# Optimization experiments

Measured on AMD Instinct MI355X. Metric: run time of the kernel, lower is better.

The kernel has to match this reference:

```python
import jax, jax.numpy as jnp
import numpy as np

N_NODES = 10000
N_EDGES = 640000
IN_FEATS = 256
H_FEATS = 128
NUM_CLASSES = 64


def _kaiming(key, shape):
    fan_in = shape[1]
    std = np.sqrt(2.0 / fan_in)
    return jax.random.normal(key, shape, dtype=jnp.float32) * std


def setup_inputs() -> dict:
    key = jax.random.key(0)
    ks = jax.random.split(key, 10)
    x = jax.random.normal(ks[0], (N_NODES, IN_FEATS), dtype=jnp.float32)
    edge_index = jax.random.randint(ks[1], (2, N_EDGES), 0, N_NODES, dtype=jnp.int64)
    return {
        "x": x,
        "edge_index": edge_index,
        "W_lin": _kaiming(ks[2], (H_FEATS, IN_FEATS)),
        "b_lin": jnp.zeros((H_FEATS,), jnp.float32),
        "Wl1": _kaiming(ks[3], (H_FEATS, H_FEATS)),
        "bl1": jnp.zeros((H_FEATS,), jnp.float32),
        "Wr1": _kaiming(ks[4], (H_FEATS, H_FEATS)),
        "Wl2": _kaiming(ks[5], (H_FEATS, H_FEATS)),
        "bl2": jnp.zeros((H_FEATS,), jnp.float32),
        "Wr2": _kaiming(ks[6], (H_FEATS, H_FEATS)),
        "W_cls": _kaiming(ks[7], (NUM_CLASSES, H_FEATS)),
    }


def _sage_conv(x, src, dst, Wl, bl, Wr, n_nodes):
    # PyG SAGEConv (mean aggr): out = lin_l(mean_{j->i} x_j) + lin_r(x_i)
    msg = x[src]                                    # [E, H] gather
    agg = jax.ops.segment_sum(msg, dst, num_segments=n_nodes)  # [N, H]
    deg = jax.ops.segment_sum(jnp.ones((src.shape[0],), x.dtype), dst,
                              num_segments=n_nodes)            # [N]
    mean = agg / jnp.maximum(deg, 1.0)[:, None]
    return mean @ Wl.T + bl + x @ Wr.T


def reference(x, edge_index, W_lin, b_lin, Wl1, bl1, Wr1, Wl2, bl2, Wr2, W_cls):
    src, dst = edge_index[0], edge_index[1]
    n = x.shape[0]
    h = jax.nn.relu(x @ W_lin.T + b_lin)            # input projection + relu
    h = _sage_conv(h, src, dst, Wl1, bl1, Wr1, n)   # sage1 (no relu: linear is truthy)
    h = _sage_conv(h, src, dst, Wl2, bl2, Wr2, n)   # sage2
    h = jax.nn.relu(h)
    return h @ W_cls.T                              # weight.mm(x.t()).t()
```

## Files before the change

### kernel.cpp

```cpp
#include <hip/hip_runtime.h>

#define NN 10000
#define HF 128
#define INF_ 256
#define CLS 64
#define CAP 128
#define RT  (NN / 16)

typedef __attribute__((ext_vector_type(8))) short short8;
typedef __attribute__((ext_vector_type(4))) float f32x4;

__device__ __forceinline__ unsigned short f2bf(float f) {
    unsigned u = __builtin_bit_cast(unsigned, f);
    u = (u + 0x7fffu + ((u >> 16) & 1u)) >> 16;
    return (unsigned short)u;
}
__device__ __forceinline__ float bfbits2f(unsigned u) {
    u <<= 16;
    return __builtin_bit_cast(float, u);
}


template <int K>
__device__ __forceinline__
void mfma_acc(int row_tile, int col0,
              const unsigned short* __restrict__ A,
              const unsigned short* __restrict__ W, f32x4 acc[4]) {
    int lane = threadIdx.x & 63;
    int m = lane & 15, quad = lane >> 4;
    const short8* ap  = (const short8*)(A + (size_t)(row_tile * 16 + m) * K + quad * 8);
    const short8* bp0 = (const short8*)(W + (size_t)(col0 +  0 + m) * K + quad * 8);
    const short8* bp1 = (const short8*)(W + (size_t)(col0 + 16 + m) * K + quad * 8);
    const short8* bp2 = (const short8*)(W + (size_t)(col0 + 32 + m) * K + quad * 8);
    const short8* bp3 = (const short8*)(W + (size_t)(col0 + 48 + m) * K + quad * 8);
#pragma unroll
    for (int k0 = 0; k0 < K; k0 += 32) {
        int ki = k0 >> 3;
        short8 a = ap[ki];
        acc[0] = __builtin_amdgcn_mfma_f32_16x16x32_bf16(a, bp0[ki], acc[0], 0, 0, 0);
        acc[1] = __builtin_amdgcn_mfma_f32_16x16x32_bf16(a, bp1[ki], acc[1], 0, 0, 0);
        acc[2] = __builtin_amdgcn_mfma_f32_16x16x32_bf16(a, bp2[ki], acc[2], 0, 0, 0);
        acc[3] = __builtin_amdgcn_mfma_f32_16x16x32_bf16(a, bp3[ki], acc[3], 0, 0, 0);
    }
}

template <bool OUT_BF16, bool RELU_OUT, bool HAS_BIAS, bool HAS_TMP>
__device__ __forceinline__
void epilogue4(int row_tile, int col0, int N, const float* __restrict__ bias,
               const float* __restrict__ tmp, f32x4 acc[4], void* __restrict__ out) {
    int lane = threadIdx.x & 63;
    int m = lane & 15, quad = lane >> 4;
#pragma unroll
    for (int c = 0; c < 4; ++c) {
        int colg = col0 + c * 16 + m;
        float bv = HAS_BIAS ? bias[colg] : 0.f;
#pragma unroll
        for (int r = 0; r < 4; ++r) {
            int rowg = row_tile * 16 + quad * 4 + r;
            float v = acc[c][r] + bv;
            if (HAS_TMP) v += tmp[(size_t)rowg * N + colg];
            if (RELU_OUT) v = fmaxf(v, 0.f);
            if (OUT_BF16) ((unsigned short*)out)[(size_t)rowg * N + colg] = f2bf(v);
            else          ((float*)out)[(size_t)rowg * N + colg] = v;
        }
    }
}

__device__ __forceinline__ short8 pack8(float4 a, float4 b) {
    short8 r;
    r[0] = (short)f2bf(a.x); r[1] = (short)f2bf(a.y);
    r[2] = (short)f2bf(a.z); r[3] = (short)f2bf(a.w);
    r[4] = (short)f2bf(b.x); r[5] = (short)f2bf(b.y);
    r[6] = (short)f2bf(b.z); r[7] = (short)f2bf(b.w);
    return r;
}

__device__ __forceinline__
void gemm1_wave(int row_tile, int col0, const float* __restrict__ x,
                const float* __restrict__ Wlin, const float* __restrict__ blin,
                unsigned short* __restrict__ h0) {
    int lane = threadIdx.x & 63;
    int m = lane & 15, quad = lane >> 4;
    const float* ar = x    + (size_t)(row_tile * 16 + m) * INF_ + quad * 8;
    const float* w0 = Wlin + (size_t)(col0 +  0 + m) * INF_ + quad * 8;
    const float* w1 = Wlin + (size_t)(col0 + 16 + m) * INF_ + quad * 8;
    const float* w2 = Wlin + (size_t)(col0 + 32 + m) * INF_ + quad * 8;
    const float* w3 = Wlin + (size_t)(col0 + 48 + m) * INF_ + quad * 8;
    f32x4 acc[4] = {};
#pragma unroll
    for (int k0 = 0; k0 < INF_; k0 += 32) {
        short8 a  = pack8(*(const float4*)(ar + k0), *(const float4*)(ar + k0 + 4));
        short8 b0 = pack8(*(const float4*)(w0 + k0), *(const float4*)(w0 + k0 + 4));
        short8 b1 = pack8(*(const float4*)(w1 + k0), *(const float4*)(w1 + k0 + 4));
        short8 b2 = pack8(*(const float4*)(w2 + k0), *(const float4*)(w2 + k0 + 4));
        short8 b3 = pack8(*(const float4*)(w3 + k0), *(const float4*)(w3 + k0 + 4));
        acc[0] = __builtin_amdgcn_mfma_f32_16x16x32_bf16(a, b0, acc[0], 0, 0, 0);
        acc[1] = __builtin_amdgcn_mfma_f32_16x16x32_bf16(a, b1, acc[1], 0, 0, 0);
        acc[2] = __builtin_amdgcn_mfma_f32_16x16x32_bf16(a, b2, acc[2], 0, 0, 0);
        acc[3] = __builtin_amdgcn_mfma_f32_16x16x32_bf16(a, b3, acc[3], 0, 0, 0);
    }
    epilogue4<true, true, true, false>(row_tile, col0, HF, blin, nullptr, acc, h0);
}

#define GB 313
#define FB 625
#define CB 288

__global__ __launch_bounds__(256)
void fused_k(const float* __restrict__ x, const float* __restrict__ Wlin,
             const float* __restrict__ blin, unsigned short* __restrict__ h0,
             const int* __restrict__ src, const int* __restrict__ dst,
             int* __restrict__ cnt, unsigned short* __restrict__ colb, int E,
             const float* __restrict__ Wl1, const float* __restrict__ Wr1,
             const float* __restrict__ Wl2, const float* __restrict__ Wr2,
             const float* __restrict__ Wcls, unsigned short* __restrict__ wb) {
    int b = blockIdx.x;
    if (b < GB) {
        int wave = threadIdx.x >> 6;
        int row_tile = b * 2 + (wave >> 1);
        if (row_tile >= RT) return;
        gemm1_wave(row_tile, (wave & 1) * 64, x, Wlin, blin, h0);
    } else if (b < GB + FB) {
        int t = (b - GB) * 256 + threadIdx.x;
        if (t * 4 < E) {
            int4 s4 = ((const int4*)src)[t];
            int4 d4 = ((const int4*)dst)[t];
            int p0 = atomicAdd(&cnt[d4.x], 1);
            int p1 = atomicAdd(&cnt[d4.y], 1);
            int p2 = atomicAdd(&cnt[d4.z], 1);
            int p3 = atomicAdd(&cnt[d4.w], 1);
            if (p0 < CAP) colb[(size_t)d4.x * CAP + p0] = (unsigned short)s4.x;
            if (p1 < CAP) colb[(size_t)d4.y * CAP + p1] = (unsigned short)s4.y;
            if (p2 < CAP) colb[(size_t)d4.z * CAP + p2] = (unsigned short)s4.z;
            if (p3 < CAP) colb[(size_t)d4.w * CAP + p3] = (unsigned short)s4.w;
        }
    } else {
        int i = (b - GB - FB) * 256 + threadIdx.x;
        const float* s; int off;
        if      (i < 16384) { s = Wl1;  off = 0; }
        else if (i < 32768) { s = Wr1;  off = 16384; }
        else if (i < 49152) { s = Wl2;  off = 32768; }
        else if (i < 65536) { s = Wr2;  off = 49152; }
        else if (i < 73728) { s = Wcls; off = 65536; }
        else return;
        wb[i] = f2bf(s[i - off]);
    }
}

#define AGB 2500

__global__ __launch_bounds__(256)
void agg_gemm_k(const unsigned short* __restrict__ h, const int* __restrict__ cnt,
                const unsigned short* __restrict__ colb, unsigned short* __restrict__ mv,
                const unsigned short* __restrict__ Wr, float* __restrict__ tmp, int n) {
    int b = blockIdx.x;
    if (b < AGB) {
        int wave = threadIdx.x >> 6;
        int lane = threadIdx.x & 63;
        int q   = lane >> 4;
        int r16 = lane & 15;
        int node = b * 4 + wave;
        if (node >= n) return;
        int deg = cnt[node];
        int c = deg > CAP ? CAP : deg;
        const unsigned short* mycol = colb + (size_t)node * CAP;
        const uint4* __restrict__ hp = (const uint4*)h;

        float a0 = 0.f, a1 = 0.f, a2 = 0.f, a3 = 0.f;
        float a4 = 0.f, a5 = 0.f, a6 = 0.f, a7 = 0.f;
        for (int base = 0; base < c; base += 64) {
            int mm = min(64, c - base);
            int colv = (base + lane < c) ? (int)mycol[base + lane] : 0;
#pragma unroll 4
            for (int jj = 0; jj < 16; ++jj) {
                if (jj * 4 >= mm) break;
                int e = jj * 4 + q;
                int s = __shfl(colv, e);
                if (e < mm) {
                    uint4 v = hp[(size_t)s * 16 + r16];
                    a0 += bfbits2f(v.x & 0xffffu); a1 += bfbits2f(v.x >> 16);
                    a2 += bfbits2f(v.y & 0xffffu); a3 += bfbits2f(v.y >> 16);
                    a4 += bfbits2f(v.z & 0xffffu); a5 += bfbits2f(v.z >> 16);
                    a6 += bfbits2f(v.w & 0xffffu); a7 += bfbits2f(v.w >> 16);
                }
            }
        }
        a0 += __shfl_xor(a0, 16); a0 += __shfl_xor(a0, 32);
        a1 += __shfl_xor(a1, 16); a1 += __shfl_xor(a1, 32);
        a2 += __shfl_xor(a2, 16); a2 += __shfl_xor(a2, 32);
        a3 += __shfl_xor(a3, 16); a3 += __shfl_xor(a3, 32);
        a4 += __shfl_xor(a4, 16); a4 += __shfl_xor(a4, 32);
        a5 += __shfl_xor(a5, 16); a5 += __shfl_xor(a5, 32);
        a6 += __shfl_xor(a6, 16); a6 += __shfl_xor(a6, 32);
        a7 += __shfl_xor(a7, 16); a7 += __shfl_xor(a7, 32);
        if (q == 0) {
            float inv = (deg > 0) ? 1.0f / (float)deg : 0.f;
            uint4 o;
            o.x = (unsigned)f2bf(a0 * inv) | ((unsigned)f2bf(a1 * inv) << 16);
            o.y = (unsigned)f2bf(a2 * inv) | ((unsigned)f2bf(a3 * inv) << 16);
            o.z = (unsigned)f2bf(a4 * inv) | ((unsigned)f2bf(a5 * inv) << 16);
            o.w = (unsigned)f2bf(a6 * inv) | ((unsigned)f2bf(a7 * inv) << 16);
            ((uint4*)mv)[(size_t)node * 16 + r16] = o;
        }
    } else {
        int bb = b - AGB;
        int wave = threadIdx.x >> 6;
        int row_tile = bb * 2 + (wave >> 1);
        if (row_tile >= RT) return;
        int col0 = (wave & 1) * 64;
        f32x4 acc[4] = {};
        mfma_acc<HF>(row_tile, col0, h, Wr, acc);
        epilogue4<false, false, false, false>(row_tile, col0, HF, nullptr, nullptr, acc, tmp);
    }
}

template <bool RELU_OUT>
__global__ __launch_bounds__(256)
void sage_fin_k(const unsigned short* __restrict__ mv, const unsigned short* __restrict__ Wl,
                const float* __restrict__ tmp, const float* __restrict__ bias,
                unsigned short* __restrict__ out) {
    int wave = threadIdx.x >> 6;
    int row_tile = blockIdx.x * 2 + (wave >> 1);
    if (row_tile >= RT) return;
    int col0 = (wave & 1) * 64;
    f32x4 acc[4] = {};
    mfma_acc<HF>(row_tile, col0, mv, Wl, acc);
    epilogue4<true, RELU_OUT, true, true>(row_tile, col0, HF, bias, tmp, acc, out);
}

__global__ __launch_bounds__(256)
void cls_gemm_k(const unsigned short* __restrict__ h2r,
                const unsigned short* __restrict__ Wc, float* __restrict__ out) {
    int wave = threadIdx.x >> 6;
    int row_tile = blockIdx.x * 4 + wave;
    if (row_tile >= RT) return;
    f32x4 acc[4] = {};
    mfma_acc<HF>(row_tile, 0, h2r, Wc, acc);
    epilogue4<false, false, false, false>(row_tile, 0, CLS, nullptr, nullptr, acc, out);
}


extern "C" void kernel_launch(void* const* d_in, const int* in_sizes, int n_in,
                              void* d_out, int out_size, void* d_ws, size_t ws_size,
                              hipStream_t stream) {
    const float* x      = (const float*)d_in[0];
    const int*   ei     = (const int*)d_in[1];
    const float* W_lin  = (const float*)d_in[2];
    const float* b_lin  = (const float*)d_in[3];
    const float* Wl1    = (const float*)d_in[4];
    const float* bl1    = (const float*)d_in[5];
    const float* Wr1    = (const float*)d_in[6];
    const float* Wl2    = (const float*)d_in[7];
    const float* bl2    = (const float*)d_in[8];
    const float* Wr2    = (const float*)d_in[9];
    const float* W_cls  = (const float*)d_in[10];
    float* out = (float*)d_out;

    const int E = in_sizes[1] / 2;
    const int* src = ei;
    const int* dst = ei + E;

    unsigned short* wb  = (unsigned short*)d_ws;
    unsigned short* wbl1 = wb;
    unsigned short* wbr1 = wb + 16384;
    unsigned short* wbl2 = wb + 32768;
    unsigned short* wbr2 = wb + 49152;
    unsigned short* wbc  = wb + 65536;
    unsigned short* h0  = wb + 73728;
    unsigned short* mv  = h0 + (size_t)NN * HF;
    unsigned short* h1  = mv + (size_t)NN * HF;
    unsigned short* h2r = h1 + (size_t)NN * HF;
    float* tmp = (float*)(h2r + (size_t)NN * HF);
    int* cnt = (int*)(tmp + (size_t)NN * HF);
    unsigned short* colb = (unsigned short*)(cnt + NN);

    hipMemsetAsync(cnt, 0, NN * sizeof(int), stream);

    fused_k<<<GB + FB + CB, 256, 0, stream>>>(
        x, W_lin, b_lin, h0, src, dst, cnt, colb, E,
        Wl1, Wr1, Wl2, Wr2, W_cls, wb);

    agg_gemm_k<<<AGB + 313, 256, 0, stream>>>(h0, cnt, colb, mv, wbr1, tmp, NN);
    sage_fin_k<false><<<(RT + 1) / 2, 256, 0, stream>>>(mv, wbl1, tmp, bl1, h1);

    agg_gemm_k<<<AGB + 313, 256, 0, stream>>>(h1, cnt, colb, mv, wbr2, tmp, NN);
    sage_fin_k<true><<<(RT + 1) / 2, 256, 0, stream>>>(mv, wbl2, tmp, bl2, h2r);

    cls_gemm_k<<<(RT + 3) / 4, 256, 0, stream>>>(h2r, wbc, out);
}
```

Baseline: 195.6 us.

## Split node aggregation across two waves and narrow GEMM tiles per wave

The neighbour aggregation now gives each node two waves, each covering half of the 128-slot adjacency list, and combines their partial sums through shared memory after a block barrier. The small GEMM kernels now assign one 16-row tile per block with fewer output columns per wave, which launches more blocks. CSR-build threads also handle one edge each instead of four. The aim is more parallelism and latency hiding for the memory-bound gather and the small GEMMs, at the cost of a block-wide sync, idle waves on low-degree nodes, and duplicated A-tile loads across waves.

```diff
diff --git a/kernel.cpp b/kernel.cpp
--- a/kernel.cpp
+++ b/kernel.cpp
@@ -21,37 +21,36 @@
 }
 
 
-template <int K>
+template <int K, int NC>
 __device__ __forceinline__
-void mfma_acc(int row_tile, int col0,
-              const unsigned short* __restrict__ A,
-              const unsigned short* __restrict__ W, f32x4 acc[4]) {
+void mfma_cols(int row_tile, int col0,
+               const unsigned short* __restrict__ A,
+               const unsigned short* __restrict__ W, f32x4* acc) {
     int lane = threadIdx.x & 63;
     int m = lane & 15, quad = lane >> 4;
-    const short8* ap  = (const short8*)(A + (size_t)(row_tile * 16 + m) * K + quad * 8);
-    const short8* bp0 = (const short8*)(W + (size_t)(col0 +  0 + m) * K + quad * 8);
-    const short8* bp1 = (const short8*)(W + (size_t)(col0 + 16 + m) * K + quad * 8);
-    const short8* bp2 = (const short8*)(W + (size_t)(col0 + 32 + m) * K + quad * 8);
-    const short8* bp3 = (const short8*)(W + (size_t)(col0 + 48 + m) * K + quad * 8);
+    const short8* ap = (const short8*)(A + (size_t)(row_tile * 16 + m) * K + quad * 8);
+    const short8* bp[NC];
+#pragma unroll
+    for (int c = 0; c < NC; ++c)
+        bp[c] = (const short8*)(W + (size_t)(col0 + c * 16 + m) * K + quad * 8);
 #pragma unroll
     for (int k0 = 0; k0 < K; k0 += 32) {
         int ki = k0 >> 3;
         short8 a = ap[ki];
-        acc[0] = __builtin_amdgcn_mfma_f32_16x16x32_bf16(a, bp0[ki], acc[0], 0, 0, 0);
-        acc[1] = __builtin_amdgcn_mfma_f32_16x16x32_bf16(a, bp1[ki], acc[1], 0, 0, 0);
-        acc[2] = __builtin_amdgcn_mfma_f32_16x16x32_bf16(a, bp2[ki], acc[2], 0, 0, 0);
-        acc[3] = __builtin_amdgcn_mfma_f32_16x16x32_bf16(a, bp3[ki], acc[3], 0, 0, 0);
-    }
-}
-
-template <bool OUT_BF16, bool RELU_OUT, bool HAS_BIAS, bool HAS_TMP>
+#pragma unroll
+        for (int c = 0; c < NC; ++c)
+            acc[c] = __builtin_amdgcn_mfma_f32_16x16x32_bf16(a, bp[c][ki], acc[c], 0, 0, 0);
+    }
+}
+
+template <int NC, bool OUT_BF16, bool RELU_OUT, bool HAS_BIAS, bool HAS_TMP>
 __device__ __forceinline__
-void epilogue4(int row_tile, int col0, int N, const float* __restrict__ bias,
-               const float* __restrict__ tmp, f32x4 acc[4], void* __restrict__ out) {
+void epilogue_n(int row_tile, int col0, int N, const float* __restrict__ bias,
+                const float* __restrict__ tmp, f32x4* acc, void* __restrict__ out) {
     int lane = threadIdx.x & 63;
     int m = lane & 15, quad = lane >> 4;
 #pragma unroll
-    for (int c = 0; c < 4; ++c) {
+    for (int c = 0; c < NC; ++c) {
         int colg = col0 + c * 16 + m;
         float bv = HAS_BIAS ? bias[colg] : 0.f;
 #pragma unroll
@@ -99,11 +98,11 @@
         acc[2] = __builtin_amdgcn_mfma_f32_16x16x32_bf16(a, b2, acc[2], 0, 0, 0);
         acc[3] = __builtin_amdgcn_mfma_f32_16x16x32_bf16(a, b3, acc[3], 0, 0, 0);
     }
-    epilogue4<true, true, true, false>(row_tile, col0, HF, blin, nullptr, acc, h0);
+    epilogue_n<4, true, true, true, false>(row_tile, col0, HF, blin, nullptr, acc, h0);
 }
 
 #define GB 313
-#define FB 625
+#define FB 2500
 #define CB 288
 
 __global__ __launch_bounds__(256)
@@ -121,18 +120,11 @@
         if (row_tile >= RT) return;
         gemm1_wave(row_tile, (wave & 1) * 64, x, Wlin, blin, h0);
     } else if (b < GB + FB) {
-        int t = (b - GB) * 256 + threadIdx.x;
-        if (t * 4 < E) {
-            int4 s4 = ((const int4*)src)[t];
-            int4 d4 = ((const int4*)dst)[t];
-            int p0 = atomicAdd(&cnt[d4.x], 1);
-            int p1 = atomicAdd(&cnt[d4.y], 1);
-            int p2 = atomicAdd(&cnt[d4.z], 1);
-            int p3 = atomicAdd(&cnt[d4.w], 1);
-            if (p0 < CAP) colb[(size_t)d4.x * CAP + p0] = (unsigned short)s4.x;
-            if (p1 < CAP) colb[(size_t)d4.y * CAP + p1] = (unsigned short)s4.y;
-            if (p2 < CAP) colb[(size_t)d4.z * CAP + p2] = (unsigned short)s4.z;
-            if (p3 < CAP) colb[(size_t)d4.w * CAP + p3] = (unsigned short)s4.w;
+        int i = (b - GB) * 256 + threadIdx.x;
+        if (i < E) {
+            int d = dst[i];
+            int pos = atomicAdd(&cnt[d], 1);
+            if (pos < CAP) colb[(size_t)d * CAP + pos] = (unsigned short)src[i];
         }
     } else {
         int i = (b - GB - FB) * 256 + threadIdx.x;
@@ -147,7 +139,7 @@
     }
 }
 
-#define AGB 2500
+#define AGB 5000
 
 __global__ __launch_bounds__(256)
 void agg_gemm_k(const unsigned short* __restrict__ h, const int* __restrict__ cnt,
@@ -155,34 +147,34 @@
                 const unsigned short* __restrict__ Wr, float* __restrict__ tmp, int n) {
     int b = blockIdx.x;
     if (b < AGB) {
+        __shared__ float part[4][8][16];
         int wave = threadIdx.x >> 6;
         int lane = threadIdx.x & 63;
-        int q   = lane >> 4;
-        int r16 = lane & 15;
-        int node = b * 4 + wave;
-        if (node >= n) return;
+        int w    = wave & 1;
+        int q    = lane >> 4;
+        int r16  = lane & 15;
+        int node = b * 2 + (wave >> 1);
         int deg = cnt[node];
         int c = deg > CAP ? CAP : deg;
-        const unsigned short* mycol = colb + (size_t)node * CAP;
+        int cw = c - w * 64;
+        cw = cw < 0 ? 0 : (cw > 64 ? 64 : cw);
+        const unsigned short* mycol = colb + (size_t)node * CAP + w * 64;
         const uint4* __restrict__ hp = (const uint4*)h;
 
         float a0 = 0.f, a1 = 0.f, a2 = 0.f, a3 = 0.f;
         float a4 = 0.f, a5 = 0.f, a6 = 0.f, a7 = 0.f;
-        for (int base = 0; base < c; base += 64) {
-            int mm = min(64, c - base);
-            int colv = (base + lane < c) ? (int)mycol[base + lane] : 0;
+        int colv = (lane < cw) ? (int)mycol[lane] : 0;
 #pragma unroll 4
-            for (int jj = 0; jj < 16; ++jj) {
-                if (jj * 4 >= mm) break;
-                int e = jj * 4 + q;
-                int s = __shfl(colv, e);
-                if (e < mm) {
-                    uint4 v = hp[(size_t)s * 16 + r16];
-                    a0 += bfbits2f(v.x & 0xffffu); a1 += bfbits2f(v.x >> 16);
-                    a2 += bfbits2f(v.y & 0xffffu); a3 += bfbits2f(v.y >> 16);
-                    a4 += bfbits2f(v.z & 0xffffu); a5 += bfbits2f(v.z >> 16);
-                    a6 += bfbits2f(v.w & 0xffffu); a7 += bfbits2f(v.w >> 16);
-                }
+        for (int jj = 0; jj < 16; ++jj) {
+            if (jj * 4 >= cw) break;
+            int e = jj * 4 + q;
+            int s = __shfl(colv, e);
+            if (e < cw) {
+                uint4 v = hp[(size_t)s * 16 + r16];
+                a0 += bfbits2f(v.x & 0xffffu); a1 += bfbits2f(v.x >> 16);
+                a2 += bfbits2f(v.y & 0xffffu); a3 += bfbits2f(v.y >> 16);
+                a4 += bfbits2f(v.z & 0xffffu); a5 += bfbits2f(v.z >> 16);
+                a6 += bfbits2f(v.w & 0xffffu); a7 += bfbits2f(v.w >> 16);
             }
         }
         a0 += __shfl_xor(a0, 16); a0 += __shfl_xor(a0, 32);
@@ -194,23 +186,36 @@
         a6 += __shfl_xor(a6, 16); a6 += __shfl_xor(a6, 32);
         a7 += __shfl_xor(a7, 16); a7 += __shfl_xor(a7, 32);
         if (q == 0) {
+            part[wave][0][r16] = a0; part[wave][1][r16] = a1;
+            part[wave][2][r16] = a2; part[wave][3][r16] = a3;
+            part[wave][4][r16] = a4; part[wave][5][r16] = a5;
+            part[wave][6][r16] = a6; part[wave][7][r16] = a7;
+        }
+        __syncthreads();
+        if (w == 0 && q == 0) {
             float inv = (deg > 0) ? 1.0f / (float)deg : 0.f;
+            float s0 = (part[wave][0][r16] + part[wave + 1][0][r16]) * inv;
+            float s1 = (part[wave][1][r16] + part[wave + 1][1][r16]) * inv;
+            float s2 = (part[wave][2][r16] + part[wave + 1][2][r16]) * inv;
+            float s3 = (part[wave][3][r16] + part[wave + 1][3][r16]) * inv;
+            float s4 = (part[wave][4][r16] + part[wave + 1][4][r16]) * inv;
+            float s5 = (part[wave][5][r16] + part[wave + 1][5][r16]) * inv;
+            float s6 = (part[wave][6][r16] + part[wave + 1][6][r16]) * inv;
+            float s7 = (part[wave][7][r16] + part[wave + 1][7][r16]) * inv;
             uint4 o;
-            o.x = (unsigned)f2bf(a0 * inv) | ((unsigned)f2bf(a1 * inv) << 16);
-            o.y = (unsigned)f2bf(a2 * inv) | ((unsigned)f2bf(a3 * inv) << 16);
-            o.z = (unsigned)f2bf(a4 * inv) | ((unsigned)f2bf(a5 * inv) << 16);
-            o.w = (unsigned)f2bf(a6 * inv) | ((unsigned)f2bf(a7 * inv) << 16);
+            o.x = (unsigned)f2bf(s0) | ((unsigned)f2bf(s1) << 16);
+            o.y = (unsigned)f2bf(s2) | ((unsigned)f2bf(s3) << 16);
+            o.z = (unsigned)f2bf(s4) | ((unsigned)f2bf(s5) << 16);
+            o.w = (unsigned)f2bf(s6) | ((unsigned)f2bf(s7) << 16);
             ((uint4*)mv)[(size_t)node * 16 + r16] = o;
         }
     } else {
-        int bb = b - AGB;
+        int row_tile = b - AGB;
         int wave = threadIdx.x >> 6;
-        int row_tile = bb * 2 + (wave >> 1);
-        if (row_tile >= RT) return;
-        int col0 = (wave & 1) * 64;
-        f32x4 acc[4] = {};
-        mfma_acc<HF>(row_tile, col0, h, Wr, acc);
-        epilogue4<false, false, false, false>(row_tile, col0, HF, nullptr, nullptr, acc, tmp);
+        f32x4 acc[2] = {};
+        mfma_cols<HF, 2>(row_tile, wave * 32, h, Wr, acc);
+        epilogue_n<2, false, false, false, false>(row_tile, wave * 32, HF,
+                                                  nullptr, nullptr, acc, tmp);
     }
 }
 
@@ -219,24 +224,23 @@
 void sage_fin_k(const unsigned short* __restrict__ mv, const unsigned short* __restrict__ Wl,
                 const float* __restrict__ tmp, const float* __restrict__ bias,
                 unsigned short* __restrict__ out) {
+    int row_tile = blockIdx.x;
     int wave = threadIdx.x >> 6;
-    int row_tile = blockIdx.x * 2 + (wave >> 1);
-    if (row_tile >= RT) return;
-    int col0 = (wave & 1) * 64;
-    f32x4 acc[4] = {};
-    mfma_acc<HF>(row_tile, col0, mv, Wl, acc);
-    epilogue4<true, RELU_OUT, true, true>(row_tile, col0, HF, bias, tmp, acc, out);
+    f32x4 acc[2] = {};
+    mfma_cols<HF, 2>(row_tile, wave * 32, mv, Wl, acc);
+    epilogue_n<2, true, RELU_OUT, true, true>(row_tile, wave * 32, HF,
+                                              bias, tmp, acc, out);
 }
 
 __global__ __launch_bounds__(256)
 void cls_gemm_k(const unsigned short* __restrict__ h2r,
                 const unsigned short* __restrict__ Wc, float* __restrict__ out) {
+    int row_tile = blockIdx.x;
     int wave = threadIdx.x >> 6;
-    int row_tile = blockIdx.x * 4 + wave;
-    if (row_tile >= RT) return;
-    f32x4 acc[4] = {};
-    mfma_acc<HF>(row_tile, 0, h2r, Wc, acc);
-    epilogue4<false, false, false, false>(row_tile, 0, CLS, nullptr, nullptr, acc, out);
+    f32x4 acc[1] = {};
+    mfma_cols<HF, 1>(row_tile, wave * 16, h2r, Wc, acc);
+    epilogue_n<1, false, false, false, false>(row_tile, wave * 16, CLS,
+                                              nullptr, nullptr, acc, out);
 }
 
 
@@ -280,11 +284,11 @@
         x, W_lin, b_lin, h0, src, dst, cnt, colb, E,
         Wl1, Wr1, Wl2, Wr2, W_cls, wb);
 
-    agg_gemm_k<<<AGB + 313, 256, 0, stream>>>(h0, cnt, colb, mv, wbr1, tmp, NN);
-    sage_fin_k<false><<<(RT + 1) / 2, 256, 0, stream>>>(mv, wbl1, tmp, bl1, h1);
-
-    agg_gemm_k<<<AGB + 313, 256, 0, stream>>>(h1, cnt, colb, mv, wbr2, tmp, NN);
-    sage_fin_k<true><<<(RT + 1) / 2, 256, 0, stream>>>(mv, wbl2, tmp, bl2, h2r);
-
-    cls_gemm_k<<<(RT + 3) / 4, 256, 0, stream>>>(h2r, wbc, out);
-}
+    agg_gemm_k<<<AGB + RT, 256, 0, stream>>>(h0, cnt, colb, mv, wbr1, tmp, NN);
+    sage_fin_k<false><<<RT, 256, 0, stream>>>(mv, wbl1, tmp, bl1, h1);
+
+    agg_gemm_k<<<AGB + RT, 256, 0, stream>>>(h1, cnt, colb, mv, wbr2, tmp, NN);
+    sage_fin_k<true><<<RT, 256, 0, stream>>>(mv, wbl2, tmp, bl2, h2r);
+
+    cls_gemm_k<<<RT, 256, 0, stream>>>(h2r, wbc, out);
+}
```

Measured after the change: 190.8 us. 2.4% less time.
